# Optimization experiments

Measured on AMD Instinct MI355X. Metric: run time of the kernel, lower is better.

## Reference

```python
import jax, jax.numpy as jnp
import numpy as np

B, T, D_MODEL = 4, 8192, 1024
D_K, D_V = 128, 128
DILATIONS = [1, 2, 4, 8]
SEG = 128                      # segment_count for every head
NORM = 1.0 / np.sqrt(D_K)      # norm_fact = 1/sqrt(d_k)
H = len(DILATIONS)


def setup_inputs() -> dict:
    key = jax.random.key(0)
    ks = jax.random.split(key, 6)
    x = jax.random.normal(ks[0], (B, T, D_MODEL), dtype=jnp.float32)
    # head weights, init like torch: randn(k, m)/sqrt(k), stacked over heads
    Wk = jax.random.normal(ks[1], (H, D_K, D_MODEL), dtype=jnp.float32) / np.sqrt(D_K)
    Wq = jax.random.normal(ks[2], (H, D_K, D_MODEL), dtype=jnp.float32) / np.sqrt(D_K)
    Wv = jax.random.normal(ks[3], (H, D_V, D_MODEL), dtype=jnp.float32) / np.sqrt(D_V)
    # output projection (concat of H heads -> d_model), torch Linear layout (out, in)
    W_out = jax.random.normal(ks[4], (D_MODEL, H * D_V), dtype=jnp.float32) / np.sqrt(H * D_V)
    b_out = jnp.zeros((D_MODEL,), dtype=jnp.float32)
    return {"x": x, "Wk": Wk, "Wq": Wq, "Wv": Wv, "W_out": W_out, "b_out": b_out}


def _head(x, wk, wq, wv, dil):
    """SingleHeadDilatedSelfAttention with padding='same', is_causal=True."""
    Bb, Tt, E = x.shape
    nb = Tt // SEG                       # attention length before dilation
    # view(B, T//seg, seg, E).permute(0,2,3,1) -> (B, seg, E, nb); dilate last dim
    xv = x.reshape(Bb, nb, SEG, E).transpose(0, 2, 3, 1)[:, :, :, ::dil]  # (B, seg, E, L)
    Q = jnp.einsum('bsel,ke->bslk', xv, wq)   # (B, seg, L, d_k)
    K = jnp.einsum('bsel,ke->bslk', xv, wk)
    V = jnp.einsum('bsel,ve->bslv', xv, wv)   # (B, seg, L, d_v)
    # KQ[b,s,n,m]: n = key position, m = query position
    KQ = jnp.einsum('bsnd,bsmd->bsnm', K, Q)
    mask = jnp.tril(jnp.ones((nb, nb), dtype=bool))[::dil, ::dil]  # (L, L)
    KQ = jnp.where(mask, KQ, -jnp.inf)
    # original applies softmax along dim 3 (the query axis) of KQ * norm_fact
    smKQ = jax.nn.softmax(KQ * NORM, axis=3)
    att = jnp.einsum('bsnm,bsnv->bsmv', smKQ, V)   # (B, seg, L, d_v)
    L = att.shape[2]
    # 'same' padding: strided scatter back to full sequence length
    out = jnp.zeros((Bb, Tt, D_V), dtype=x.dtype)
    out = out.at[:, ::dil, :].set(att.reshape(Bb, SEG * L, D_V))
    return out


def reference(x, Wk, Wq, Wv, W_out, b_out):
    heads = [_head(x, Wk[h], Wq[h], Wv[h], DILATIONS[h]) for h in range(H)]
    cat = jnp.concatenate(heads, axis=-1)            # (B, T, H*d_v)
    return cat @ W_out.T + b_out                     # (B, T, d_model)
```

## Files before the change

### kernel.cpp

```cpp
#include <hip/hip_runtime.h>
#include <cstdint>
#include <cstddef>

typedef __attribute__((ext_vector_type(8))) short bf16x8;
typedef __attribute__((ext_vector_type(4))) float f32x4;

__device__ __forceinline__ unsigned short f2bf(float f) {
  union { float f; uint32_t u; } v; v.f = f;
  uint32_t r = v.u + 0x7fffu + ((v.u >> 16) & 1u);
  return (unsigned short)(r >> 16);
}
__device__ __forceinline__ float bf2f(unsigned short u) {
  union { uint32_t u; float f; } v; v.u = ((uint32_t)u) << 16;
  return v.f;
}

__device__ __forceinline__ size_t head_off(int h) {
  return (size_t)65536 * ((h == 0) ? 0 : (h == 1) ? 64 : (h == 2) ? 96 : 112);
}

__global__ void k_cvt(const float* __restrict__ src, unsigned short* __restrict__ dst, int n4) {
  int i = blockIdx.x * 256 + threadIdx.x;
  if (i < n4) {
    float4 f = ((const float4*)src)[i];
    ushort4 u;
    u.x = f2bf(f.x); u.y = f2bf(f.y); u.z = f2bf(f.z); u.w = f2bf(f.w);
    ((ushort4*)dst)[i] = u;
  }
}

__global__ void k_cvt_w(const float* __restrict__ Wq, const float* __restrict__ Wk,
                        const float* __restrict__ Wv, unsigned short* __restrict__ dst) {
  int row = blockIdx.x;
  int h = row / 384, j = row % 384;
  const float* src = (j < 128) ? (Wq + (size_t)(h * 128 + j) * 1024)
                   : (j < 256) ? (Wk + (size_t)(h * 128 + j - 128) * 1024)
                               : (Wv + (size_t)(h * 128 + j - 256) * 1024);
  int e = threadIdx.x * 4;
  float4 f = *(const float4*)(src + e);
  ushort4 u;
  u.x = f2bf(f.x); u.y = f2bf(f.y); u.z = f2bf(f.z); u.w = f2bf(f.w);
  *(ushort4*)(dst + (size_t)row * 1024 + e) = u;
}

__global__ __launch_bounds__(256) void k_qkv(
    const unsigned short* __restrict__ xbf,
    const unsigned short* __restrict__ wbf,
    unsigned short* __restrict__ qws,
    unsigned short* __restrict__ kws,
    unsigned short* __restrict__ vws) {
  int gx = blockIdx.x, gy = blockIdx.y;
  int h, base;
  if (gx < 256)      { h = 0; base = 0; }
  else if (gx < 384) { h = 1; base = 256; }
  else if (gx < 448) { h = 2; base = 384; }
  else               { h = 3; base = 448; }
  int L = 64 >> h, dil = 1 << h;
  int inner = gx - base;
  int b = inner >> (6 - h);
  int l = inner & (L - 1);
  const unsigned short* Abase = xbf + ((size_t)(b * 8192 + l * dil * 128)) * 1024;
  const unsigned short* Bbase = wbf + ((size_t)(h * 384 + gy * 128)) * 1024;

  __shared__ unsigned short As[128][72];
  __shared__ unsigned short Bs[128][72];

  int tid = threadIdx.x;
  int lane = tid & 63, wave = tid >> 6;
  int wm = wave >> 1, wn = wave & 1;
  int li = lane & 15, lk8 = (lane >> 4) << 3;

  f32x4 acc[4][4] = {};

  int sr = tid >> 1, sc = (tid & 1) * 32;
  const unsigned short* Ag = Abase + (size_t)sr * 1024 + sc;
  const unsigned short* Bg = Bbase + (size_t)sr * 1024 + sc;

  for (int kc = 0; kc < 1024; kc += 64) {
    bf16x8 av[4], bv[4];
#pragma unroll
    for (int i = 0; i < 4; ++i) {
      av[i] = *(const bf16x8*)(Ag + kc + i * 8);
      bv[i] = *(const bf16x8*)(Bg + kc + i * 8);
    }
    __syncthreads();
#pragma unroll
    for (int i = 0; i < 4; ++i) {
      *(bf16x8*)&As[sr][sc + i * 8] = av[i];
      *(bf16x8*)&Bs[sr][sc + i * 8] = bv[i];
    }
    __syncthreads();
#pragma unroll
    for (int kk = 0; kk < 2; ++kk) {
      int k0 = kk * 32 + lk8;
      bf16x8 af[4], bfv[4];
#pragma unroll
      for (int mf = 0; mf < 4; ++mf)
        af[mf] = *(const bf16x8*)&As[wm * 64 + mf * 16 + li][k0];
#pragma unroll
      for (int nf = 0; nf < 4; ++nf)
        bfv[nf] = *(const bf16x8*)&Bs[wn * 64 + nf * 16 + li][k0];
#pragma unroll
      for (int mf = 0; mf < 4; ++mf)
#pragma unroll
        for (int nf = 0; nf < 4; ++nf)
          acc[mf][nf] = __builtin_amdgcn_mfma_f32_16x16x32_bf16(af[mf], bfv[nf], acc[mf][nf], 0, 0, 0);
    }
  }
  unsigned short* dst = ((gy == 0) ? qws : (gy == 1) ? kws : vws) + head_off(h);
  int ib = (lane >> 4) * 4;
#pragma unroll
  for (int mf = 0; mf < 4; ++mf) {
#pragma unroll
    for (int nf = 0; nf < 4; ++nf) {
#pragma unroll
      for (int rg = 0; rg < 4; ++rg) {
        int s = wm * 64 + mf * 16 + ib + rg;
        int j = wn * 64 + nf * 16 + li;
        dst[((size_t)((b * 128 + s) * L + l)) * 128 + j] = f2bf(acc[mf][nf][rg]);
      }
    }
  }
}

__global__ __launch_bounds__(256) void k_attn(
    const unsigned short* __restrict__ qws,
    const unsigned short* __restrict__ kws,
    const unsigned short* __restrict__ vws,
    unsigned short* __restrict__ att) {
  int h = blockIdx.y;
  int bs = blockIdx.x;
  int L = 64 >> h;
  size_t off = head_off(h) + (size_t)bs * L * 128;
  const unsigned short* Qg = qws + off;
  const unsigned short* Kg = kws + off;
  const unsigned short* Vg = vws + off;

  __shared__ unsigned short Ks[64 * 128];
  __shared__ unsigned short Q2[64 * 128];
  __shared__ float S[64][65];

  int tid = threadIdx.x;
  int n8 = (L * 128) / 8;
  for (int i = tid; i < n8; i += 256) {
    ((bf16x8*)Ks)[i] = ((const bf16x8*)Kg)[i];
    ((bf16x8*)Q2)[i] = ((const bf16x8*)Qg)[i];
  }
  __syncthreads();
  for (int p = tid; p < L * L; p += 256) {
    int n = p >> (6 - h), m = p & (L - 1);
    if (m <= n) {
      const uint32_t* kr = (const uint32_t*)(Ks + n * 128);
      const uint32_t* qr = (const uint32_t*)(Q2 + m * 128);
      float a = 0.f;
#pragma unroll 8
      for (int d = 0; d < 64; ++d) {
        uint32_t ku = kr[d], qu = qr[d];
        union { uint32_t u; float f; } kl, kh, ql, qh;
        kl.u = ku << 16; kh.u = ku & 0xffff0000u;
        ql.u = qu << 16; qh.u = qu & 0xffff0000u;
        a += kl.f * ql.f + kh.f * qh.f;
      }
      S[n][m] = a * 0.08838834764831845f;
    }
  }
  __syncthreads();
  if (tid < L) {
    int n = tid;
    float mx = -1e30f;
    for (int m = 0; m <= n; ++m) mx = fmaxf(mx, S[n][m]);
    float sum = 0.f;
    for (int m = 0; m <= n; ++m) { float e = __expf(S[n][m] - mx); S[n][m] = e; sum += e; }
    float inv = 1.f / sum;
    for (int m = 0; m <= n; ++m) S[n][m] *= inv;
  }
  __syncthreads();
  for (int i = tid; i < n8; i += 256)
    ((bf16x8*)Q2)[i] = ((const bf16x8*)Vg)[i];
  __syncthreads();
  for (int o = tid; o < L * 128; o += 256) {
    int m = o >> 7, vv = o & 127;
    float a = 0.f;
    for (int n = m; n < L; ++n)
      a += S[n][m] * bf2f(Q2[n * 128 + vv]);
    att[off + (size_t)m * 128 + vv] = f2bf(a);
  }
}

__global__ __launch_bounds__(256) void k_out(
    const unsigned short* __restrict__ att,
    const unsigned short* __restrict__ wout,
    const float* __restrict__ bout,
    float* __restrict__ out) {
  int mt = blockIdx.x, nt = blockIdx.y;
  int row0 = mt * 128;

  __shared__ unsigned short As[128][72];
  __shared__ unsigned short Bs[128][72];

  int tid = threadIdx.x;
  int lane = tid & 63, wave = tid >> 6;
  int wm = wave >> 1, wn = wave & 1;
  int li = lane & 15, lk8 = (lane >> 4) << 3;

  f32x4 acc[4][4] = {};

  int sr = tid >> 1, sc = (tid & 1) * 32;
  int rowg = row0 + sr;
  int b = rowg >> 13, t = rowg & 8191;
  const unsigned short* Bg = wout + (size_t)(nt * 128 + sr) * 512 + sc;
  const bf16x8 ZV = {0, 0, 0, 0, 0, 0, 0, 0};

  for (int kc = 0; kc < 512; kc += 64) {
    int c0 = kc + sc;
    int hd = c0 >> 7, v0 = c0 & 127;
    int dil = 1 << hd, Lh = 64 >> hd;
    bf16x8 av[4], bv[4];
    if ((t & (dil - 1)) == 0) {
      int j = t >> hd;
      int s = j >> (6 - hd), l = j & (Lh - 1);
      const unsigned short* Ag = att + head_off(hd)
          + ((size_t)((b * 128 + s) * Lh + l)) * 128 + v0;
#pragma unroll
      for (int i = 0; i < 4; ++i) av[i] = *(const bf16x8*)(Ag + i * 8);
    } else {
#pragma unroll
      for (int i = 0; i < 4; ++i) av[i] = ZV;
    }
#pragma unroll
    for (int i = 0; i < 4; ++i) bv[i] = *(const bf16x8*)(Bg + kc + i * 8);
    __syncthreads();
#pragma unroll
    for (int i = 0; i < 4; ++i) {
      *(bf16x8*)&As[sr][sc + i * 8] = av[i];
      *(bf16x8*)&Bs[sr][sc + i * 8] = bv[i];
    }
    __syncthreads();
#pragma unroll
    for (int kk = 0; kk < 2; ++kk) {
      int k0 = kk * 32 + lk8;
      bf16x8 af[4], bfv[4];
#pragma unroll
      for (int mf = 0; mf < 4; ++mf)
        af[mf] = *(const bf16x8*)&As[wm * 64 + mf * 16 + li][k0];
#pragma unroll
      for (int nf = 0; nf < 4; ++nf)
        bfv[nf] = *(const bf16x8*)&Bs[wn * 64 + nf * 16 + li][k0];
#pragma unroll
      for (int mf = 0; mf < 4; ++mf)
#pragma unroll
        for (int nf = 0; nf < 4; ++nf)
          acc[mf][nf] = __builtin_amdgcn_mfma_f32_16x16x32_bf16(af[mf], bfv[nf], acc[mf][nf], 0, 0, 0);
    }
  }
  int ib = (lane >> 4) * 4;
#pragma unroll
  for (int mf = 0; mf < 4; ++mf) {
#pragma unroll
    for (int nf = 0; nf < 4; ++nf) {
      int col = nt * 128 + wn * 64 + nf * 16 + li;
      float bo = bout[col];
#pragma unroll
      for (int rg = 0; rg < 4; ++rg) {
        int r = row0 + wm * 64 + mf * 16 + ib + rg;
        out[(size_t)r * 1024 + col] = acc[mf][nf][rg] + bo;
      }
    }
  }
}

extern "C" void kernel_launch(void* const* d_in, const int* in_sizes, int n_in,
                              void* d_out, int out_size, void* d_ws, size_t ws_size,
                              hipStream_t stream) {
  const float* x  = (const float*)d_in[0];
  const float* Wk = (const float*)d_in[1];
  const float* Wq = (const float*)d_in[2];
  const float* Wv = (const float*)d_in[3];
  const float* Wo = (const float*)d_in[4];
  const float* bo = (const float*)d_in[5];
  float* out = (float*)d_out;
  char* ws = (char*)d_ws;
  unsigned short* xbf  = (unsigned short*)(ws);
  unsigned short* wbf  = (unsigned short*)(ws + 67108864);
  unsigned short* wobf = (unsigned short*)(ws + 70254592);
  unsigned short* qws  = (unsigned short*)(ws + 71303168);
  unsigned short* kws  = (unsigned short*)(ws + 87031808);
  unsigned short* vws  = (unsigned short*)(ws + 102760448);
  unsigned short* attw = (unsigned short*)(ws + 118489088);

  k_cvt<<<dim3(32768), dim3(256), 0, stream>>>(x, xbf, 8388608);
  k_cvt_w<<<dim3(1536), dim3(256), 0, stream>>>(Wq, Wk, Wv, wbf);
  k_cvt<<<dim3(512), dim3(256), 0, stream>>>(Wo, wobf, 131072);
  k_qkv<<<dim3(480, 3), dim3(256), 0, stream>>>(xbf, wbf, qws, kws, vws);
  k_attn<<<dim3(512, 4), dim3(256), 0, stream>>>(qws, kws, vws, attw);
  k_out<<<dim3(256, 8), dim3(256), 0, stream>>>(attw, wobf, bo, out);
}
```

Measured before the change: 454.6 us.

## Rewrite attention kernel with MFMA and pack short-head segments into 64-row tiles

Replaces the scalar dot-product attention with bf16 MFMA for both QK^T and PV. Segments of the dilated heads (L<64) are packed into full 64-row tiles using a block-diagonal causal mask, so the grid becomes one flat launch of 960 blocks instead of 2048 partly idle ones. Softmax now runs in registers with wave shuffles, and P and a transposed V are staged in LDS. The trade-off is wasted MFMA work on masked off-diagonal entries and a strided transposed write of V into LDS.

```diff
diff --git a/kernel.cpp b/kernel.cpp
--- a/kernel.cpp
+++ b/kernel.cpp
@@ -128,62 +128,113 @@
     const unsigned short* __restrict__ kws,
     const unsigned short* __restrict__ vws,
     unsigned short* __restrict__ att) {
-  int h = blockIdx.y;
-  int bs = blockIdx.x;
+  int bx = blockIdx.x;
+  int h, inst;
+  if (bx < 512)      { h = 0; inst = bx; }
+  else if (bx < 768) { h = 1; inst = bx - 512; }
+  else if (bx < 896) { h = 2; inst = bx - 768; }
+  else               { h = 3; inst = bx - 896; }
+  int lgL = 6 - h;
   int L = 64 >> h;
-  size_t off = head_off(h) + (size_t)bs * L * 128;
-  const unsigned short* Qg = qws + off;
-  const unsigned short* Kg = kws + off;
-  const unsigned short* Vg = vws + off;
-
-  __shared__ unsigned short Ks[64 * 128];
-  __shared__ unsigned short Q2[64 * 128];
-  __shared__ float S[64][65];
+  int Lm1 = L - 1;
+  int bpb = 128 >> h;
+  int b = inst / bpb;
+  int s0 = (inst % bpb) << h;
+  size_t off0 = head_off(h) + ((size_t)(b * 128 + s0) * L) * 128;
+  const unsigned short* Qg = qws + off0;
+  const unsigned short* Kg = kws + off0;
+  const unsigned short* Vg = vws + off0;
+  unsigned short* Og = att + off0;
+
+  __shared__ unsigned short PT[64][72];
+  __shared__ unsigned short VtL[128][72];
 
   int tid = threadIdx.x;
-  int n8 = (L * 128) / 8;
-  for (int i = tid; i < n8; i += 256) {
-    ((bf16x8*)Ks)[i] = ((const bf16x8*)Kg)[i];
-    ((bf16x8*)Q2)[i] = ((const bf16x8*)Qg)[i];
+  int lane = tid & 63, w = tid >> 6;
+  int li = lane & 15, q = lane >> 4;
+  int lk8 = q << 3;
+
+#pragma unroll
+  for (int c = 0; c < 4; ++c) {
+    int u = tid + c * 256;
+    int n = u & 63, vblk = u >> 6;
+    bf16x8 ve = *(const bf16x8*)(Vg + n * 128 + vblk * 8);
+#pragma unroll
+    for (int j = 0; j < 8; ++j)
+      VtL[vblk * 8 + j][n] = (unsigned short)ve[j];
+  }
+
+  f32x4 sacc[4] = {};
+  int nrow = 16 * w + li;
+  for (int kc = 0; kc < 4; ++kc) {
+    int d0 = kc * 32 + lk8;
+    bf16x8 af = *(const bf16x8*)(Kg + nrow * 128 + d0);
+#pragma unroll
+    for (int mt = 0; mt < 4; ++mt) {
+      bf16x8 bfq = *(const bf16x8*)(Qg + (mt * 16 + li) * 128 + d0);
+      sacc[mt] = __builtin_amdgcn_mfma_f32_16x16x32_bf16(af, bfq, sacc[mt], 0, 0, 0);
+    }
+  }
+
+  float sv[4][4];
+#pragma unroll
+  for (int mt = 0; mt < 4; ++mt)
+#pragma unroll
+    for (int r = 0; r < 4; ++r) {
+      int n = 16 * w + 4 * q + r;
+      int m = mt * 16 + li;
+      bool valid = ((m >> lgL) == (n >> lgL)) && ((m & Lm1) <= (n & Lm1));
+      sv[mt][r] = valid ? sacc[mt][r] * 0.08838834764831845f : -1e30f;
+    }
+  float inv[4];
+#pragma unroll
+  for (int r = 0; r < 4; ++r) {
+    float m0 = fmaxf(fmaxf(sv[0][r], sv[1][r]), fmaxf(sv[2][r], sv[3][r]));
+#pragma unroll
+    for (int d = 1; d < 16; d <<= 1)
+      m0 = fmaxf(m0, __shfl_xor(m0, d, 64));
+    float s0 = 0.f;
+#pragma unroll
+    for (int mt = 0; mt < 4; ++mt) {
+      sv[mt][r] = __expf(sv[mt][r] - m0);
+      s0 += sv[mt][r];
+    }
+#pragma unroll
+    for (int d = 1; d < 16; d <<= 1)
+      s0 += __shfl_xor(s0, d, 64);
+    inv[r] = 1.f / s0;
+  }
+
+#pragma unroll
+  for (int mt = 0; mt < 4; ++mt) {
+    ushort4 pk;
+    pk.x = f2bf(sv[mt][0] * inv[0]);
+    pk.y = f2bf(sv[mt][1] * inv[1]);
+    pk.z = f2bf(sv[mt][2] * inv[2]);
+    pk.w = f2bf(sv[mt][3] * inv[3]);
+    *(ushort4*)&PT[mt * 16 + li][16 * w + 4 * q] = pk;
   }
   __syncthreads();
-  for (int p = tid; p < L * L; p += 256) {
-    int n = p >> (6 - h), m = p & (L - 1);
-    if (m <= n) {
-      const uint32_t* kr = (const uint32_t*)(Ks + n * 128);
-      const uint32_t* qr = (const uint32_t*)(Q2 + m * 128);
-      float a = 0.f;
-#pragma unroll 8
-      for (int d = 0; d < 64; ++d) {
-        uint32_t ku = kr[d], qu = qr[d];
-        union { uint32_t u; float f; } kl, kh, ql, qh;
-        kl.u = ku << 16; kh.u = ku & 0xffff0000u;
-        ql.u = qu << 16; qh.u = qu & 0xffff0000u;
-        a += kl.f * ql.f + kh.f * qh.f;
-      }
-      S[n][m] = a * 0.08838834764831845f;
-    }
-  }
-  __syncthreads();
-  if (tid < L) {
-    int n = tid;
-    float mx = -1e30f;
-    for (int m = 0; m <= n; ++m) mx = fmaxf(mx, S[n][m]);
-    float sum = 0.f;
-    for (int m = 0; m <= n; ++m) { float e = __expf(S[n][m] - mx); S[n][m] = e; sum += e; }
-    float inv = 1.f / sum;
-    for (int m = 0; m <= n; ++m) S[n][m] *= inv;
-  }
-  __syncthreads();
-  for (int i = tid; i < n8; i += 256)
-    ((bf16x8*)Q2)[i] = ((const bf16x8*)Vg)[i];
-  __syncthreads();
-  for (int o = tid; o < L * 128; o += 256) {
-    int m = o >> 7, vv = o & 127;
-    float a = 0.f;
-    for (int n = m; n < L; ++n)
-      a += S[n][m] * bf2f(Q2[n * 128 + vv]);
-    att[off + (size_t)m * 128 + vv] = f2bf(a);
+
+  f32x4 oacc[8] = {};
+#pragma unroll
+  for (int ks = 0; ks < 2; ++ks) {
+    int n0 = ks * 32 + lk8;
+    bf16x8 af = *(const bf16x8*)&PT[16 * w + li][n0];
+#pragma unroll
+    for (int vt = 0; vt < 8; ++vt) {
+      bf16x8 bfv = *(const bf16x8*)&VtL[vt * 16 + li][n0];
+      oacc[vt] = __builtin_amdgcn_mfma_f32_16x16x32_bf16(af, bfv, oacc[vt], 0, 0, 0);
+    }
+  }
+#pragma unroll
+  for (int vt = 0; vt < 8; ++vt) {
+#pragma unroll
+    for (int r = 0; r < 4; ++r) {
+      int m = 16 * w + 4 * q + r;
+      int v = vt * 16 + li;
+      Og[m * 128 + v] = f2bf(oacc[vt][r]);
+    }
   }
 }
 
@@ -292,6 +343,6 @@
   k_cvt_w<<<dim3(1536), dim3(256), 0, stream>>>(Wq, Wk, Wv, wbf);
   k_cvt<<<dim3(512), dim3(256), 0, stream>>>(Wo, wobf, 131072);
   k_qkv<<<dim3(480, 3), dim3(256), 0, stream>>>(xbf, wbf, qws, kws, vws);
-  k_attn<<<dim3(512, 4), dim3(256), 0, stream>>>(qws, kws, vws, attw);
+  k_attn<<<dim3(960), dim3(256), 0, stream>>>(qws, kws, vws, attw);
   k_out<<<dim3(256, 8), dim3(256), 0, stream>>>(attw, wobf, bo, out);
 }
```

After: 372.3 us. 1.22x faster.
